# Kernel optimization log

Measured on AMD Instinct MI355X. Metric: run time of the kernel, lower is better.

Reference implementation:

```python
import jax, jax.numpy as jnp
import numpy as np

B, S, D, H = 2, 2048, 1024, 16
DK = D // H


def setup_inputs() -> dict:
    key = jax.random.key(0)
    ks = jax.random.split(key, 9)
    def xavier(k, shape):
        fan_in, fan_out = shape[1], shape[0]
        lim = jnp.sqrt(6.0 / (fan_in + fan_out))
        return jax.random.uniform(k, shape, jnp.float32, -lim, lim)
    x = jax.random.normal(ks[0], (B, S, D), jnp.float32)
    mask = jnp.ones((B, 1, S), jnp.int32)
    Wq = xavier(ks[1], (D, D)); bq = jnp.zeros((D,), jnp.float32)
    Wk = xavier(ks[2], (D, D)); bk = jnp.zeros((D,), jnp.float32)
    Wv = xavier(ks[3], (D, D)); bv = jnp.zeros((D,), jnp.float32)
    Wo = xavier(ks[4], (D, D)); bo = jnp.zeros((D,), jnp.float32)
    return {"x": x, "mask": mask, "Wq": Wq, "bq": bq, "Wk": Wk, "bk": bk,
            "Wv": Wv, "bv": bv, "Wo": Wo, "bo": bo}


def reference(x, mask, Wq, bq, Wk, bk, Wv, bv, Wo, bo):
    # Linear layers use torch convention y = x @ W.T + b
    q = (x @ Wq.T + bq).reshape(B, S, H, DK).transpose(0, 2, 1, 3)  # [B,H,S,DK]
    k = (x @ Wk.T + bk).reshape(B, S, H, DK).transpose(0, 2, 1, 3)
    v = (x @ Wv.T + bv).reshape(B, S, H, DK).transpose(0, 2, 1, 3)
    scores = jnp.einsum('bhqd,bhkd->bhqk', q, k) / jnp.sqrt(jnp.float32(DK))
    m = mask[:, None, :, :]  # unsqueeze(1): broadcast over heads -> [B,1,1,S]
    scores = jnp.where(m == 0, jnp.float32(-1e9), scores)
    p = jax.nn.softmax(scores, axis=-1)  # dropout p=0.0 -> identity
    ctx = jnp.einsum('bhqk,bhkd->bhqd', p, v)
    ctx = ctx.transpose(0, 2, 1, 3).reshape(B, S, D)
    return ctx @ Wo.T + bo
```

## Files before the change

### kernel.cpp

```cpp
#include <hip/hip_runtime.h>
#include <hip/hip_bf16.h>
#include <math.h>

#define Bn 2
#define Sn 2048
#define Dn 1024
#define Hn 16
#define DKn 64
#define BHS (Bn * Hn * Sn)

using fragb  = __attribute__((ext_vector_type(8))) short;
using frag16 = __attribute__((ext_vector_type(8))) _Float16;
using f4     = __attribute__((ext_vector_type(4))) float;

__device__ __forceinline__ short f2bf(float f) {
    union { float f; unsigned u; } v; v.f = f;
    unsigned r = v.u + 0x7FFF + ((v.u >> 16) & 1);
    return (short)(r >> 16);
}
__device__ __forceinline__ unsigned short f2h(float f) {
    _Float16 h = (_Float16)f;
    unsigned short s; __builtin_memcpy(&s, &h, 2); return s;
}

#define GLOAD(gptr, lptr)                                                     \
    __builtin_amdgcn_global_load_lds(                                         \
        (const __attribute__((address_space(1))) unsigned int*)(const void*)(gptr), \
        (__attribute__((address_space(3))) unsigned int*)(void*)(lptr), 16, 0, 0)

#define NX (Bn * Sn * Dn)
#define NW (Dn * Dn)
#define NF4 ((NX + 4 * NW) / 4)

__global__ __launch_bounds__(256) void prep(
    const float* __restrict__ x,  const float* __restrict__ Wq,
    const float* __restrict__ Wk, const float* __restrict__ Wv,
    const float* __restrict__ Wo, const int* __restrict__ mask,
    short* __restrict__ xh,
    short* __restrict__ Wqh, short* __restrict__ Wkh,
    short* __restrict__ Wvh, short* __restrict__ Woh,
    short* __restrict__ mfb)
{
    int i = blockIdx.x * 256 + threadIdx.x;
    if (i < NF4) {
        int e = i << 2;
        const float* src; short* dst; int j;
        if (e < NX)               { src = x;  dst = xh;  j = e; }
        else if (e < NX + NW)     { src = Wq; dst = Wqh; j = e - NX; }
        else if (e < NX + 2 * NW) { src = Wk; dst = Wkh; j = e - NX - NW; }
        else if (e < NX + 3 * NW) { src = Wv; dst = Wvh; j = e - NX - 2 * NW; }
        else                      { src = Wo; dst = Woh; j = e - NX - 3 * NW; }
        float4 v = *(const float4*)(src + j);
        ushort4 o;
        o.x = f2h(v.x); o.y = f2h(v.y); o.z = f2h(v.z); o.w = f2h(v.w);
        *(ushort4*)(dst + j) = o;
    } else {
        int j = (i - NF4) << 2;
        if (j < Bn * Sn) {
            int4 m = *(const int4*)(mask + j);
            ushort4 o;
            o.x = m.x ? 0x3F80 : 0; o.y = m.y ? 0x3F80 : 0;
            o.z = m.z ? 0x3F80 : 0; o.w = m.w ? 0x3F80 : 0;
            *(ushort4*)(mfb + j) = o;
        }
    }
}

__global__ __launch_bounds__(256) void gemm_qkv(
    const short* __restrict__ A,
    const short* __restrict__ W0, const float* __restrict__ b0,
    const short* __restrict__ W1, const float* __restrict__ b1,
    const short* __restrict__ W2, const float* __restrict__ b2,
    const int* __restrict__ mask,
    short* __restrict__ Qb, short* __restrict__ Kb, short* __restrict__ Vtb)
{
    __shared__ __align__(16) short As[128 * 32];
    __shared__ __align__(16) short Bs[128 * 32];

    const int tid  = threadIdx.x;
    const int wave = tid >> 6;
    const int lane = tid & 63;
    const int quad = lane >> 4;
    const int l16  = lane & 15;
    const int wm   = wave >> 1;
    const int wn   = wave & 1;

    const int m0   = blockIdx.y * 128;
    const int n0   = blockIdx.x * 128;
    const int widx = n0 >> 10;
    const int nl0  = n0 & 1023;

    const short* Wp   = widx == 0 ? W0 : (widx == 1 ? W1 : W2);
    const float* bias = widx == 0 ? b0 : (widx == 1 ? b1 : b2);

    f4 acc[4][4];
    #pragma unroll
    for (int i = 0; i < 4; i++)
        #pragma unroll
        for (int j = 0; j < 4; j++) {
            acc[i][j][0] = 0.f; acc[i][j][1] = 0.f;
            acc[i][j][2] = 0.f; acc[i][j][3] = 0.f;
        }

    const int K = Dn;
    const int r0  = tid >> 2,         kc0 = (tid & 3) * 8;
    const int r1  = (tid + 256) >> 2;
    const short* Ar0 = A  + (size_t)(m0 + r0) * K + kc0;
    const short* Ar1 = A  + (size_t)(m0 + r1) * K + kc0;
    const short* Br0 = Wp + (size_t)(nl0 + r0) * K + kc0;
    const short* Br1 = Wp + (size_t)(nl0 + r1) * K + kc0;

    for (int k0 = 0; k0 < K; k0 += 32) {
        __syncthreads();
        GLOAD(Ar0 + k0, &As[(wave * 64) * 8]);
        GLOAD(Ar1 + k0, &As[(256 + wave * 64) * 8]);
        GLOAD(Br0 + k0, &Bs[(wave * 64) * 8]);
        GLOAD(Br1 + k0, &Bs[(256 + wave * 64) * 8]);
        __syncthreads();

        frag16 a[4], b[4];
        #pragma unroll
        for (int mi = 0; mi < 4; mi++)
            a[mi] = *(const frag16*)&As[(wm * 64 + mi * 16 + l16) * 32 + quad * 8];
        #pragma unroll
        for (int ni = 0; ni < 4; ni++)
            b[ni] = *(const frag16*)&Bs[(wn * 64 + ni * 16 + l16) * 32 + quad * 8];
        #pragma unroll
        for (int mi = 0; mi < 4; mi++)
            #pragma unroll
            for (int ni = 0; ni < 4; ni++)
                acc[mi][ni] = __builtin_amdgcn_mfma_f32_16x16x32_f16(
                    a[mi], b[ni], acc[mi][ni], 0, 0, 0);
    }

    const float QSCALE = 0.125f * 1.44269504088896340736f;

    #pragma unroll
    for (int mi = 0; mi < 4; mi++) {
        #pragma unroll
        for (int ni = 0; ni < 4; ni++) {
            int nl = nl0 + wn * 64 + ni * 16 + l16;
            float bv = bias[nl];
            #pragma unroll
            for (int r = 0; r < 4; r++) {
                int m = m0 + wm * 64 + mi * 16 + quad * 4 + r;
                float v = acc[mi][ni][r] + bv;
                int b  = m >> 11, s = m & (Sn - 1);
                int h  = nl >> 6, dk = nl & 63;
                if (widx == 0)
                    Qb[((size_t)(b * Hn + h) * Sn + s) * DKn + dk] = f2bf(v * QSCALE);
                else if (widx == 1)
                    Kb[((size_t)(b * Hn + h) * Sn + s) * DKn + dk] = f2bf(v);
                else {
                    float mv = (float)mask[b * Sn + s];
                    Vtb[((size_t)(b * Hn + h) * DKn + dk) * Sn + s] = f2bf(v * mv);
                }
            }
        }
    }
}

__global__ __launch_bounds__(256) void gemm_out(
    const short* __restrict__ A, const short* __restrict__ Wp,
    const float* __restrict__ bias, float* __restrict__ outf)
{
    __shared__ __align__(16) short As[64 * 32];
    __shared__ __align__(16) short Bs[128 * 32];

    const int tid  = threadIdx.x;
    const int wave = tid >> 6;
    const int lane = tid & 63;
    const int quad = lane >> 4;
    const int l16  = lane & 15;
    const int wm   = wave >> 1;
    const int wn   = wave & 1;

    const int m0 = blockIdx.y * 64;
    const int n0 = blockIdx.x * 128;

    f4 acc[2][4];
    #pragma unroll
    for (int i = 0; i < 2; i++)
        #pragma unroll
        for (int j = 0; j < 4; j++) {
            acc[i][j][0] = 0.f; acc[i][j][1] = 0.f;
            acc[i][j][2] = 0.f; acc[i][j][3] = 0.f;
        }

    const int K = Dn;
    const int r0  = tid >> 2,         kc0 = (tid & 3) * 8;
    const int r1  = (tid + 256) >> 2;
    const short* Ar0 = A  + (size_t)(m0 + r0) * K + kc0;
    const short* Br0 = Wp + (size_t)(n0 + r0) * K + kc0;
    const short* Br1 = Wp + (size_t)(n0 + r1) * K + kc0;

    for (int k0 = 0; k0 < K; k0 += 32) {
        __syncthreads();
        GLOAD(Ar0 + k0, &As[(wave * 64) * 8]);
        GLOAD(Br0 + k0, &Bs[(wave * 64) * 8]);
        GLOAD(Br1 + k0, &Bs[(256 + wave * 64) * 8]);
        __syncthreads();

        frag16 a[2], b[4];
        #pragma unroll
        for (int mi = 0; mi < 2; mi++)
            a[mi] = *(const frag16*)&As[(wm * 32 + mi * 16 + l16) * 32 + quad * 8];
        #pragma unroll
        for (int ni = 0; ni < 4; ni++)
            b[ni] = *(const frag16*)&Bs[(wn * 64 + ni * 16 + l16) * 32 + quad * 8];
        #pragma unroll
        for (int mi = 0; mi < 2; mi++)
            #pragma unroll
            for (int ni = 0; ni < 4; ni++)
                acc[mi][ni] = __builtin_amdgcn_mfma_f32_16x16x32_f16(
                    a[mi], b[ni], acc[mi][ni], 0, 0, 0);
    }

    #pragma unroll
    for (int mi = 0; mi < 2; mi++) {
        #pragma unroll
        for (int ni = 0; ni < 4; ni++) {
            int nl = n0 + wn * 64 + ni * 16 + l16;
            float bv = bias[nl];
            #pragma unroll
            for (int r = 0; r < 4; r++) {
                int m = m0 + wm * 32 + mi * 16 + quad * 4 + r;
                outf[(size_t)m * Dn + nl] = acc[mi][ni][r] + bv;
            }
        }
    }
}

#define LP  72

__global__ __launch_bounds__(256) void attn_mfma(
    const short* __restrict__ Qb, const short* __restrict__ Kb,
    const short* __restrict__ Vtb, const short* __restrict__ mfb,
    float* __restrict__ ctxp0, float* __restrict__ ctxp1,
    float* __restrict__ lp)
{
    __shared__ __align__(16) short Ks[64 * 64];
    __shared__ __align__(16) short Vs[64 * 64];
    __shared__ short Ps[4][32 * LP];
    __shared__ __align__(16) short mfs[64];

    const int tid  = threadIdx.x;
    const int wave = tid >> 6;
    const int lane = tid & 63;
    const int quad = lane >> 4;
    const int l16  = lane & 15;

    const int split = blockIdx.x & 1;
    const int rest  = blockIdx.x >> 1;
    const int qt  = rest & 15;
    const int bhh = rest >> 4;
    const int b   = bhh >> 4;
    const int h   = bhh & 15;

    fragb qf[2][2];
    #pragma unroll
    for (int w = 0; w < 2; w++) {
        int qrow = qt * 128 + wave * 32 + w * 16 + l16;
        const short* qptr = Qb + ((size_t)bhh * Sn + qrow) * DKn + quad * 8;
        qf[w][0] = *(const fragb*)(qptr);
        qf[w][1] = *(const fragb*)(qptr + 32);
    }

    f4 ctx[2][4];
    #pragma unroll
    for (int w = 0; w < 2; w++)
        #pragma unroll
        for (int dt = 0; dt < 4; dt++) {
            ctx[w][dt][0] = 0.f; ctx[w][dt][1] = 0.f;
            ctx[w][dt][2] = 0.f; ctx[w][dt][3] = 0.f;
        }
    f4 lacc[2];
    lacc[0][0] = 0.f; lacc[0][1] = 0.f; lacc[0][2] = 0.f; lacc[0][3] = 0.f;
    lacc[1] = lacc[0];

    const int lr = lane >> 3;
    const int sc = ((lane & 7) ^ lr) * 8;
    const short* Kg = Kb  + (size_t)bhh * Sn * DKn;
    const short* Vg = Vtb + (size_t)bhh * DKn * Sn;
    const short* mg = mfb + (size_t)b * Sn;

    const short* Ksrc = Kg + (size_t)(wave * 16 + lr) * DKn + sc;
    const short* Vsrc = Vg + (size_t)(wave * 16 + lr) * Sn + sc;

    const int c0 = ((quad ^ (l16 & 7)) * 8);

    const int kt0 = split * 16;
    for (int kt = kt0; kt < kt0 + 16; kt++) {
        __syncthreads();
        GLOAD(Ksrc + (size_t)kt * 4096,             &Ks[(wave * 16) * 64]);
        GLOAD(Ksrc + (size_t)kt * 4096 + 8 * DKn,   &Ks[(wave * 16 + 8) * 64]);
        GLOAD(Vsrc + (size_t)kt * 64,               &Vs[(wave * 16) * 64]);
        GLOAD(Vsrc + (size_t)kt * 64 + 8 * Sn,      &Vs[(wave * 16 + 8) * 64]);
        if (tid < 8)
            *(uint4*)&mfs[tid * 8] = *(const uint4*)(mg + kt * 64 + tid * 8);
        __syncthreads();

        #pragma unroll
        for (int t = 0; t < 4; t++) {
            fragb k0 = *(const fragb*)&Ks[(t * 16 + l16) * 64 + c0];
            fragb k1 = *(const fragb*)&Ks[(t * 16 + l16) * 64 + (c0 ^ 32)];
            #pragma unroll
            for (int w = 0; w < 2; w++) {
                f4 a; a[0] = 0.f; a[1] = 0.f; a[2] = 0.f; a[3] = 0.f;
                a = __builtin_amdgcn_mfma_f32_16x16x32_bf16(k0, qf[w][0], a, 0, 0, 0);
                a = __builtin_amdgcn_mfma_f32_16x16x32_bf16(k1, qf[w][1], a, 0, 0, 0);
                unsigned u0 = __float_as_uint(__builtin_amdgcn_exp2f(a[0]));
                unsigned u1 = __float_as_uint(__builtin_amdgcn_exp2f(a[1]));
                unsigned u2 = __float_as_uint(__builtin_amdgcn_exp2f(a[2]));
                unsigned u3 = __float_as_uint(__builtin_amdgcn_exp2f(a[3]));
                uint2 pw;
                pw.x = __builtin_amdgcn_perm(u1, u0, 0x07060302u);
                pw.y = __builtin_amdgcn_perm(u3, u2, 0x07060302u);
                *(uint2*)&Ps[wave][(w * 16 + l16) * LP + 16 * t + quad * 4] = pw;
            }
        }

        fragb p[2][2];
        #pragma unroll
        for (int w = 0; w < 2; w++) {
            p[w][0] = *(const fragb*)&Ps[wave][(w * 16 + l16) * LP + quad * 8];
            p[w][1] = *(const fragb*)&Ps[wave][(w * 16 + l16) * LP + quad * 8 + 32];
        }
        fragb m0 = *(const fragb*)&mfs[quad * 8];
        fragb m1 = *(const fragb*)&mfs[quad * 8 + 32];
        #pragma unroll
        for (int w = 0; w < 2; w++) {
            lacc[w] = __builtin_amdgcn_mfma_f32_16x16x32_bf16(p[w][0], m0, lacc[w], 0, 0, 0);
            lacc[w] = __builtin_amdgcn_mfma_f32_16x16x32_bf16(p[w][1], m1, lacc[w], 0, 0, 0);
        }
        #pragma unroll
        for (int dt = 0; dt < 4; dt++) {
            fragb v0 = *(const fragb*)&Vs[(dt * 16 + l16) * 64 + c0];
            fragb v1 = *(const fragb*)&Vs[(dt * 16 + l16) * 64 + (c0 ^ 32)];
            #pragma unroll
            for (int w = 0; w < 2; w++) {
                ctx[w][dt] = __builtin_amdgcn_mfma_f32_16x16x32_bf16(p[w][0], v0, ctx[w][dt], 0, 0, 0);
                ctx[w][dt] = __builtin_amdgcn_mfma_f32_16x16x32_bf16(p[w][1], v1, ctx[w][dt], 0, 0, 0);
            }
        }
    }

    float* cp  = split ? ctxp1 : ctxp0;
    float* lpp = lp + (size_t)split * BHS;
    #pragma unroll
    for (int w = 0; w < 2; w++)
        #pragma unroll
        for (int r = 0; r < 4; r++) {
            int row = qt * 128 + wave * 32 + w * 16 + quad * 4 + r;
            if (l16 == 0) lpp[(size_t)bhh * Sn + row] = lacc[w][r];
            #pragma unroll
            for (int dt = 0; dt < 4; dt++)
                cp[((size_t)(b * Sn + row)) * Dn + h * DKn + dt * 16 + l16] =
                    ctx[w][dt][r];
        }
}

__global__ __launch_bounds__(256) void reduce_ctx(
    const float* __restrict__ c0, const float* __restrict__ c1,
    const float* __restrict__ lp, short* __restrict__ Ch)
{
    int i4 = blockIdx.x * 256 + threadIdx.x;
    int e    = i4 << 2;
    int brow = e >> 10;
    int d    = e & 1023;
    int b    = brow >> 11;
    int row  = brow & (Sn - 1);
    int h    = d >> 6;
    size_t li = (size_t)(b * Hn + h) * Sn + row;
    float l = lp[li] + lp[BHS + li];
    float inv = 1.f / l;
    float4 v0 = ((const float4*)c0)[i4];
    float4 v1 = ((const float4*)c1)[i4];
    ushort4 o;
    o.x = f2h((v0.x + v1.x) * inv);
    o.y = f2h((v0.y + v1.y) * inv);
    o.z = f2h((v0.z + v1.z) * inv);
    o.w = f2h((v0.w + v1.w) * inv);
    ((ushort4*)Ch)[i4] = o;
}

extern "C" void kernel_launch(void* const* d_in, const int* in_sizes, int n_in,
                              void* d_out, int out_size, void* d_ws, size_t ws_size,
                              hipStream_t stream) {
    const float* x    = (const float*)d_in[0];
    const int*   mask = (const int*)d_in[1];
    const float* Wq   = (const float*)d_in[2];
    const float* bq   = (const float*)d_in[3];
    const float* Wk   = (const float*)d_in[4];
    const float* bk   = (const float*)d_in[5];
    const float* Wv   = (const float*)d_in[6];
    const float* bv   = (const float*)d_in[7];
    const float* Wo   = (const float*)d_in[8];
    const float* bo   = (const float*)d_in[9];
    float* out = (float*)d_out;

    char* ws = (char*)d_ws;
    const size_t MB = 1024u * 1024u;
    short* xh    = (short*)(ws + 0 * MB);
    short* Wqh   = (short*)(ws + 8 * MB);
    short* Wkh   = (short*)(ws + 10 * MB);
    short* Wvh   = (short*)(ws + 12 * MB);
    short* Qb    = (short*)(ws + 16 * MB);
    short* Kb    = (short*)(ws + 24 * MB);
    short* Vtb   = (short*)(ws + 32 * MB);
    float* ctxp0 = (float*)(ws + 0 * MB);
    float* ctxp1 = (float*)(ws + 40 * MB);
    short* Woh   = (short*)(ws + 56 * MB);
    float* lp    = (float*)(ws + 58 * MB);
    short* mfb   = (short*)(ws + 59 * MB);
    short* Ch    = (short*)(ws + 60 * MB);

    const int PRE = NF4 + (Bn * Sn) / 4;
    prep<<<(PRE + 255) / 256, 256, 0, stream>>>(
        x, Wq, Wk, Wv, Wo, mask, xh, Wqh, Wkh, Wvh, Woh, mfb);

    gemm_qkv<<<dim3(24, 32), 256, 0, stream>>>(
        xh, Wqh, bq, Wkh, bk, Wvh, bv, mask, Qb, Kb, Vtb);

    attn_mfma<<<dim3(Bn * Hn * (Sn / 128) * 2), 256, 0, stream>>>(
        Qb, Kb, Vtb, mfb, ctxp0, ctxp1, lp);

    reduce_ctx<<<dim3(NX / 4 / 256), 256, 0, stream>>>(ctxp0, ctxp1, lp, Ch);

    gemm_out<<<dim3(8, 64), 256, 0, stream>>>(Ch, Woh, bo, out);
}
```

Before: 213.0 us.

## Load QKV GEMM fragments directly from global with register double buffering; add MFMA priority hints

The QKV projection GEMM no longer stages A and W tiles through LDS with two barriers per k-step. Each lane now loads its MFMA fragments straight from global memory into registers, double-buffered so the next k-slice loads while the current one feeds MFMAs. The attention kernel also wraps its MFMA blocks in s_setprio to raise wave priority during matrix work. The GEMM change drops LDS traffic and syncs, but each wave now fetches its tiles without sharing across waves, which raises global/L2 traffic and register use.

```diff
diff --git a/kernel.cpp b/kernel.cpp
--- a/kernel.cpp
+++ b/kernel.cpp
@@ -74,9 +74,6 @@
     const int* __restrict__ mask,
     short* __restrict__ Qb, short* __restrict__ Kb, short* __restrict__ Vtb)
 {
-    __shared__ __align__(16) short As[128 * 32];
-    __shared__ __align__(16) short Bs[128 * 32];
-
     const int tid  = threadIdx.x;
     const int wave = tid >> 6;
     const int lane = tid & 63;
@@ -102,36 +99,44 @@
             acc[i][j][2] = 0.f; acc[i][j][3] = 0.f;
         }
 
-    const int K = Dn;
-    const int r0  = tid >> 2,         kc0 = (tid & 3) * 8;
-    const int r1  = (tid + 256) >> 2;
-    const short* Ar0 = A  + (size_t)(m0 + r0) * K + kc0;
-    const short* Ar1 = A  + (size_t)(m0 + r1) * K + kc0;
-    const short* Br0 = Wp + (size_t)(nl0 + r0) * K + kc0;
-    const short* Br1 = Wp + (size_t)(nl0 + r1) * K + kc0;
-
-    for (int k0 = 0; k0 < K; k0 += 32) {
-        __syncthreads();
-        GLOAD(Ar0 + k0, &As[(wave * 64) * 8]);
-        GLOAD(Ar1 + k0, &As[(256 + wave * 64) * 8]);
-        GLOAD(Br0 + k0, &Bs[(wave * 64) * 8]);
-        GLOAD(Br1 + k0, &Bs[(256 + wave * 64) * 8]);
-        __syncthreads();
-
-        frag16 a[4], b[4];
-        #pragma unroll
-        for (int mi = 0; mi < 4; mi++)
-            a[mi] = *(const frag16*)&As[(wm * 64 + mi * 16 + l16) * 32 + quad * 8];
-        #pragma unroll
-        for (int ni = 0; ni < 4; ni++)
-            b[ni] = *(const frag16*)&Bs[(wn * 64 + ni * 16 + l16) * 32 + quad * 8];
-        #pragma unroll
-        for (int mi = 0; mi < 4; mi++)
-            #pragma unroll
-            for (int ni = 0; ni < 4; ni++)
-                acc[mi][ni] = __builtin_amdgcn_mfma_f32_16x16x32_f16(
-                    a[mi], b[ni], acc[mi][ni], 0, 0, 0);
-    }
+    const short* Apt[4];
+    const short* Bpt[4];
+    #pragma unroll
+    for (int mi = 0; mi < 4; mi++)
+        Apt[mi] = A  + (size_t)(m0  + wm * 64 + mi * 16 + l16) * Dn + quad * 8;
+    #pragma unroll
+    for (int ni = 0; ni < 4; ni++)
+        Bpt[ni] = Wp + (size_t)(nl0 + wn * 64 + ni * 16 + l16) * Dn + quad * 8;
+
+#define LOADSET(AF, BF, kk) do {                                              \
+    _Pragma("unroll")                                                         \
+    for (int mi = 0; mi < 4; mi++)                                            \
+        AF[mi] = *(const frag16*)(Apt[mi] + (kk));                            \
+    _Pragma("unroll")                                                         \
+    for (int ni = 0; ni < 4; ni++)                                            \
+        BF[ni] = *(const frag16*)(Bpt[ni] + (kk));                            \
+} while (0)
+
+#define MFMASET(AF, BF) do {                                                  \
+    _Pragma("unroll")                                                         \
+    for (int mi = 0; mi < 4; mi++)                                            \
+        _Pragma("unroll")                                                     \
+        for (int ni = 0; ni < 4; ni++)                                        \
+            acc[mi][ni] = __builtin_amdgcn_mfma_f32_16x16x32_f16(             \
+                AF[mi], BF[ni], acc[mi][ni], 0, 0, 0);                        \
+} while (0)
+
+    frag16 a0[4], b0f[4], a1[4], b1f[4];
+    LOADSET(a0, b0f, 0);
+    for (int k = 0; k < 960; k += 64) {
+        LOADSET(a1, b1f, k + 32);
+        MFMASET(a0, b0f);
+        LOADSET(a0, b0f, k + 64);
+        MFMASET(a1, b1f);
+    }
+    LOADSET(a1, b1f, 992);
+    MFMASET(a0, b0f);
+    MFMASET(a1, b1f);
 
     const float QSCALE = 0.125f * 1.44269504088896340736f;
 
@@ -307,8 +312,10 @@
             #pragma unroll
             for (int w = 0; w < 2; w++) {
                 f4 a; a[0] = 0.f; a[1] = 0.f; a[2] = 0.f; a[3] = 0.f;
+                __builtin_amdgcn_s_setprio(1);
                 a = __builtin_amdgcn_mfma_f32_16x16x32_bf16(k0, qf[w][0], a, 0, 0, 0);
                 a = __builtin_amdgcn_mfma_f32_16x16x32_bf16(k1, qf[w][1], a, 0, 0, 0);
+                __builtin_amdgcn_s_setprio(0);
                 unsigned u0 = __float_as_uint(__builtin_amdgcn_exp2f(a[0]));
                 unsigned u1 = __float_as_uint(__builtin_amdgcn_exp2f(a[1]));
                 unsigned u2 = __float_as_uint(__builtin_amdgcn_exp2f(a[2]));
@@ -328,6 +335,7 @@
         }
         fragb m0 = *(const fragb*)&mfs[quad * 8];
         fragb m1 = *(const fragb*)&mfs[quad * 8 + 32];
+        __builtin_amdgcn_s_setprio(1);
         #pragma unroll
         for (int w = 0; w < 2; w++) {
             lacc[w] = __builtin_amdgcn_mfma_f32_16x16x32_bf16(p[w][0], m0, lacc[w], 0, 0, 0);
@@ -343,6 +351,7 @@
                 ctx[w][dt] = __builtin_amdgcn_mfma_f32_16x16x32_bf16(p[w][1], v1, ctx[w][dt], 0, 0, 0);
             }
         }
+        __builtin_amdgcn_s_setprio(0);
     }
 
     float* cp  = split ? ctxp1 : ctxp0;
```

Result: slower. 299.9 us (+40.8%).
